# Kernel tuning notes

Hardware: AMD Instinct MI355X
Metric: run time of the kernel (lower is better)

Reference implementation:

```python
import jax, jax.numpy as jnp
import numpy as np

V, D, NH, HD, FF, NL, NLOOPS = 1056, 320, 5, 64, 864, 6, 8
CAP, EPS, THETA = 0.8, 1e-6, 10000.0
B, S = 8, 2048


def rmsnorm(x, w):
    return w * (x * jax.lax.rsqrt(jnp.mean(x * x, axis=-1, keepdims=True) + EPS))


def rotate_half(x):
    x1, x2 = jnp.split(x, 2, axis=-1)
    return jnp.concatenate([-x2, x1], axis=-1)


def rope_tables(seq_len):
    freqs = 1.0 / (THETA ** (jnp.arange(0, HD, 2, dtype=jnp.float32) / HD))  # [HD/2]
    t = jnp.arange(seq_len, dtype=jnp.float32)
    f = jnp.outer(t, freqs)                      # [S, HD/2]
    f = jnp.concatenate([f, f], axis=-1)         # [S, HD]
    return jnp.cos(f), jnp.sin(f)


def setup_inputs() -> dict:
    key = jax.random.key(0)
    ks = jax.random.split(key, 12)
    std = 0.02
    inp = {
        "input_ids": jax.random.randint(ks[0], (B, S), 0, V),
        "iteration": 0,
        "embedding": jax.random.normal(ks[1], (V, D), jnp.float32),
        "iter_emb": jax.random.normal(ks[2], (NLOOPS, D), jnp.float32),
        "attn_norm_w": jnp.ones((NL, D), jnp.float32),
        "Wqkv": jax.random.normal(ks[3], (NL, 3 * D, D), jnp.float32) * std,
        "wo_w": jax.random.normal(ks[4], (NL, D, D), jnp.float32) * std,
        "router_w": jax.random.normal(ks[5], (NL, D), jnp.float32) * std,
        "mlp_norm_w": jnp.ones((NL, D), jnp.float32),
        "gate_w": jax.random.normal(ks[6], (NL, FF, D), jnp.float32) * std,
        "up_w": jax.random.normal(ks[7], (NL, FF, D), jnp.float32) * std,
        "down_w": jax.random.normal(ks[8], (NL, D, FF), jnp.float32) * std,
        "final_norm_w": jnp.ones((D,), jnp.float32),
    }
    return inp


def reference(input_ids, iteration, embedding, iter_emb, attn_norm_w, Wqkv, wo_w,
              router_w, mlp_norm_w, gate_w, up_w, down_w, final_norm_w):
    batch, seq = input_ids.shape
    k = max(1, int(seq * CAP))
    cos, sin = rope_tables(seq)                 # [S, HD]
    cos4 = cos[None, :, None, :]                # [1,S,1,HD]
    sin4 = sin[None, :, None, :]

    x = embedding[input_ids]                    # [B,S,D]
    if iteration < NLOOPS:
        x = x + iter_emb[iteration][None, None, :]

    causal = jnp.tril(jnp.ones((seq, seq), dtype=bool))
    bidx = jnp.arange(batch)[:, None]           # [B,1]

    for l in range(NL):
        # --- attention block ---
        h = rmsnorm(x, attn_norm_w[l])
        qkv = (h @ Wqkv[l].T).reshape(batch, seq, 3, NH, HD)
        q, kk, v = qkv[:, :, 0], qkv[:, :, 1], qkv[:, :, 2]   # [B,S,H,HD]
        q = q * cos4 + rotate_half(q) * sin4
        kk = kk * cos4 + rotate_half(kk) * sin4
        q, kk, v = (t.transpose(0, 2, 1, 3) for t in (q, kk, v))  # [B,H,S,HD]
        scores = jnp.einsum("bhqd,bhkd->bhqk", q, kk) / np.sqrt(HD)
        scores = jnp.where(causal, scores, -jnp.inf)
        attn = jax.nn.softmax(scores, axis=-1)
        out = jnp.einsum("bhqk,bhkd->bhqd", attn, v)
        out = out.transpose(0, 2, 1, 3).reshape(batch, seq, D)
        x = x + out @ wo_w[l].T

        # --- MoD router + SwiGLU MLP on selected tokens ---
        probs = jax.nn.sigmoid(x @ router_w[l])            # [B,S]
        topk_probs, topk_idx = jax.lax.top_k(probs, k)     # [B,K]
        sel = jnp.take_along_axis(x, topk_idx[:, :, None], axis=1)  # [B,K,D]
        hs = rmsnorm(sel, mlp_norm_w[l])
        gate = jax.nn.silu(hs @ gate_w[l].T) * (hs @ up_w[l].T)
        mlp = (gate @ down_w[l].T) * topk_probs[:, :, None]         # [B,K,D]
        x = x.at[bidx, topk_idx].add(mlp)                  # unique idx: add == scatter-set+residual

    return rmsnorm(x, final_norm_w)
```

## Files before the change

kernel.cpp:

```cpp
#include <hip/hip_runtime.h>
#include <hip/hip_bf16.h>
#include <math.h>

#define VSZ 1056
#define DD 320
#define NH 5
#define HD 64
#define FF 864
#define NL 6
#define NLOOPS 8
#define BB 8
#define SL 2048
#define KK 1638
#define EPSF 1e-6f

typedef _Float16 f16x8 __attribute__((ext_vector_type(8)));
typedef _Float16 f16x4 __attribute__((ext_vector_type(4)));
typedef float floatx16 __attribute__((ext_vector_type(16)));

__device__ inline void gll16(const void* g, void* l) {
    __builtin_amdgcn_global_load_lds((const __attribute__((address_space(1))) void*)g,
                                     (__attribute__((address_space(3))) void*)l, 16, 0, 0);
}

__global__ __launch_bounds__(256) void cast4_kernel(const float* __restrict__ s,
        _Float16* __restrict__ d, int n4) {
    int i = blockIdx.x * 256 + threadIdx.x;
    if (i >= n4) return;
    float4 v = ((const float4*)s)[i];
    f16x4 o = { (_Float16)v.x, (_Float16)v.y, (_Float16)v.z, (_Float16)v.w };
    *(f16x4*)(d + (size_t)i * 4) = o;
}

__global__ __launch_bounds__(256) void rope_init_kernel(float2* __restrict__ tab) {
    int i = blockIdx.x * 256 + threadIdx.x;
    int s = i >> 5, j = i & 31;
    float freq = exp2f(-(float)j * 0.4152410118609203f);
    float ang = (float)s * freq;
    tab[i] = make_float2(cosf(ang), sinf(ang));
}

__global__ __launch_bounds__(256) void embed_kernel(const int* __restrict__ ids,
        const int* __restrict__ iter, const float* __restrict__ emb,
        const float* __restrict__ iter_emb, float* __restrict__ x) {
    int i = blockIdx.x * 256 + threadIdx.x;
    int d = i % DD, bs = i / DD;
    float v = emb[(size_t)ids[bs] * DD + d];
    int it = iter[0];
    if (it < NLOOPS) v += iter_emb[it * DD + d];
    x[i] = v;
}

template<typename OT>
__global__ __launch_bounds__(256) void rmsnorm_kernel(const float* __restrict__ x,
        const float* __restrict__ w, OT* __restrict__ out, int nrows) {
    int row = blockIdx.x * 4 + (threadIdx.x >> 6);
    int lane = threadIdx.x & 63;
    if (row >= nrows) return;
    const float* xr = x + (size_t)row * DD;
    float v[5]; float ss = 0.f;
#pragma unroll
    for (int i = 0; i < 5; ++i) { v[i] = xr[lane + i * 64]; ss += v[i] * v[i]; }
#pragma unroll
    for (int o = 32; o > 0; o >>= 1) ss += __shfl_xor(ss, o);
    float r = rsqrtf(ss * (1.f / DD) + EPSF);
    OT* orow = out + (size_t)row * DD;
#pragma unroll
    for (int i = 0; i < 5; ++i) orow[lane + i * 64] = (OT)(w[lane + i * 64] * v[i] * r);
}

__global__ __launch_bounds__(256) void gather_rmsnorm_kernel(const float* __restrict__ x,
        const int* __restrict__ tkidx, const float* __restrict__ w,
        _Float16* __restrict__ out, int nrows) {
    int row = blockIdx.x * 4 + (threadIdx.x >> 6);
    int lane = threadIdx.x & 63;
    if (row >= nrows) return;
    int b = row / KK;
    int t = tkidx[row];
    const float* xr = x + ((size_t)b * SL + t) * DD;
    float v[5]; float ss = 0.f;
#pragma unroll
    for (int i = 0; i < 5; ++i) { v[i] = xr[lane + i * 64]; ss += v[i] * v[i]; }
#pragma unroll
    for (int o = 32; o > 0; o >>= 1) ss += __shfl_xor(ss, o);
    float r = rsqrtf(ss * (1.f / DD) + EPSF);
    _Float16* orow = out + (size_t)row * DD;
#pragma unroll
    for (int i = 0; i < 5; ++i) orow[lane + i * 64] = (_Float16)(w[lane + i * 64] * v[i] * r);
}

__global__ __launch_bounds__(256) void router_kernel(const float* __restrict__ x,
        const float* __restrict__ rw, float* __restrict__ probs, int nrows) {
    int row = blockIdx.x * 4 + (threadIdx.x >> 6);
    int lane = threadIdx.x & 63;
    if (row >= nrows) return;
    const float* xr = x + (size_t)row * DD;
    float ss = 0.f;
#pragma unroll
    for (int i = 0; i < 5; ++i) ss += xr[lane + i * 64] * rw[lane + i * 64];
#pragma unroll
    for (int o = 32; o > 0; o >>= 1) ss += __shfl_xor(ss, o);
    if (lane == 0) probs[row] = 1.f / (1.f + __expf(-ss));
}

__global__ __launch_bounds__(1024) void topk_kernel(const float* __restrict__ probs,
        int* __restrict__ tkidx, float* __restrict__ tkprob) {
    __shared__ int hist[256];
    __shared__ int scn[256];
    __shared__ int outc;
    __shared__ int s_digit, s_rem;
    int b = blockIdx.x, tid = threadIdx.x;
    unsigned long long k0, k1;
    {
        unsigned int f0 = __float_as_uint(probs[b * SL + tid]);
        unsigned int f1 = __float_as_uint(probs[b * SL + tid + 1024]);
        k0 = ((unsigned long long)f0 << 32) | (unsigned int)(2047 - tid);
        k1 = ((unsigned long long)f1 << 32) | (unsigned int)(2047 - (tid + 1024));
    }
    if (tid == 0) outc = 0;
    unsigned long long prefix = 0, pmask = 0;
    int target = KK;
    for (int shift = 56; shift >= 0; shift -= 8) {
        if (tid < 256) hist[tid] = 0;
        __syncthreads();
        bool a0 = (k0 & pmask) == prefix;
        bool a1 = (k1 & pmask) == prefix;
        int d0 = (int)((k0 >> shift) & 255);
        int d1 = (int)((k1 >> shift) & 255);
        if (a0) atomicAdd(&hist[d0], 1);
        if (a1) atomicAdd(&hist[d1], 1);
        __syncthreads();
        if (tid < 64) {
            int h0 = hist[tid * 4], h1 = hist[tid * 4 + 1];
            int h2 = hist[tid * 4 + 2], h3 = hist[tid * 4 + 3];
            int s3 = h3, s2 = h2 + s3, s1 = h1 + s2, s0 = h0 + s1;
            int s = s0;
#pragma unroll
            for (int off = 1; off < 64; off <<= 1) {
                int v = __shfl_down(s, off);
                if (tid + off >= 64) v = 0;
                s += v;
            }
            int A = s - s0;
            scn[tid * 4]     = s0 + A;
            scn[tid * 4 + 1] = s1 + A;
            scn[tid * 4 + 2] = s2 + A;
            scn[tid * 4 + 3] = s3 + A;
        }
        __syncthreads();
        if (tid < 256 && hist[tid] > 0) {
            int S = scn[tid];
            int Sgt = S - hist[tid];
            if (Sgt < target && target <= S) { s_digit = tid; s_rem = target - Sgt; }
        }
        __syncthreads();
        int dsel = s_digit, rem = s_rem;
        bool full = (rem == hist[dsel]);
        if (a0 && (d0 > dsel || (full && d0 == dsel))) {
            int s = atomicAdd(&outc, 1);
            tkidx[b * KK + s] = 2047 - (int)(k0 & 0xffffffffu);
            tkprob[b * KK + s] = __uint_as_float((unsigned int)(k0 >> 32));
        }
        if (a1 && (d1 > dsel || (full && d1 == dsel))) {
            int s = atomicAdd(&outc, 1);
            tkidx[b * KK + s] = 2047 - (int)(k1 & 0xffffffffu);
            tkprob[b * KK + s] = __uint_as_float((unsigned int)(k1 >> 32));
        }
        if (full) break;
        target = rem;
        prefix |= ((unsigned long long)dsel) << shift;
        pmask  |= ((unsigned long long)255) << shift;
        __syncthreads();
    }
}

__global__ __launch_bounds__(256) void prep_kernel(const _Float16* __restrict__ qkv,
        const float2* __restrict__ ropet,
        _Float16* __restrict__ Qh, _Float16* __restrict__ Kt, _Float16* __restrict__ Vt) {
    __shared__ _Float16 vt[64][72];
    int tid = threadIdx.x;
    int t = blockIdx.x, h = blockIdx.y, b = blockIdx.z;
    int bh = b * NH + h;
    int c = tid >> 5;
    int slb = tid & 31;
    const float QS = 0.125f * 1.44269504088896341f;
#pragma unroll
    for (int half = 0; half < 2; ++half) {
        int sl = half * 32 + slb;
        int s = t * 64 + sl;
        size_t rbase = ((size_t)(b * SL + s) * 3) * (NH * 64) + h * 64;
        f16x8 qv = *(const f16x8*)(qkv + rbase + c * 8);
        f16x8 qp = *(const f16x8*)(qkv + rbase + (c ^ 4) * 8);
        f16x8 kv = *(const f16x8*)(qkv + rbase + NH * 64 + c * 8);
        f16x8 kp = *(const f16x8*)(qkv + rbase + NH * 64 + (c ^ 4) * 8);
        f16x8 vv = *(const f16x8*)(qkv + rbase + 2 * NH * 64 + c * 8);
        const float2* rp = ropet + (size_t)s * 32 + (c & 3) * 8;
        f16x8 qo, ko;
#pragma unroll
        for (int j = 0; j < 8; ++j) {
            int d = c * 8 + j;
            float2 cs = rp[j];
            float cc = cs.x, sn = cs.y;
            float a = (float)qv[j], p = (float)qp[j];
            float ka = (float)kv[j], kb2 = (float)kp[j];
            float qr = (d < 32) ? a * cc - p * sn : a * cc + p * sn;
            float kr = (d < 32) ? ka * cc - kb2 * sn : ka * cc + kb2 * sn;
            qo[j] = (_Float16)(qr * QS);
            ko[j] = (_Float16)kr;
        }
        *(f16x8*)(Qh + ((size_t)bh * SL + s) * 64 + c * 8) = qo;
        *(f16x8*)(Kt + (((size_t)bh * 32 + t) * 8 + c) * 512 + sl * 8) = ko;
        *(f16x8*)(&vt[sl][c * 8]) = vv;
    }
    __syncthreads();
#pragma unroll
    for (int gg = 0; gg < 2; ++gg) {
        int oo = tid * 16 + gg * 8;
        int kc = oo >> 9;
        int d = (oo >> 3) & 63;
        f16x8 vo;
#pragma unroll
        for (int j = 0; j < 8; ++j) {
            int key = (kc >> 1) * 16 + (j & 3) + 8 * (j >> 2) + 4 * (kc & 1);
            vo[j] = vt[key][d];
        }
        *(f16x8*)(Vt + (((size_t)bh * 32 + t) * 8 + kc) * 512 + d * 8) = vo;
    }
}

__global__ __launch_bounds__(256, 2) void attn_mfma(const _Float16* __restrict__ Qh,
        const _Float16* __restrict__ Kt, const _Float16* __restrict__ Vt,
        _Float16* __restrict__ attn_out) {
    __shared__ float red[4][32][32];
    __shared__ float msh[4][32];
    __shared__ float lsh[4][32];
    int tid = threadIdx.x;
    int w = tid >> 6;
    int lane = tid & 63;
    int l31 = lane & 31, h5 = lane >> 5;
    int g = blockIdx.x;
    int j = g >> 3;
    int bh = (g & 7) + 8 * (j >> 6);
    int qt = 63 - (j & 63);
    int b = bh / NH, h = bh % NH;
    int nt = (qt >> 1) + 1;
    int qw = qt * 32;
    int myq = qw + l31;

    f16x8 qf[4];
    const _Float16* qrow = Qh + ((size_t)bh * SL + myq) * 64;
#pragma unroll
    for (int kd = 0; kd < 4; ++kd) qf[kd] = *(const f16x8*)(qrow + kd * 16 + h5 * 8);

    const _Float16* Kb = Kt + (size_t)bh * 32 * 4096;
    const _Float16* Vb = Vt + (size_t)bh * 32 * 4096;

    floatx16 O0, O1;
#pragma unroll
    for (int r = 0; r < 16; ++r) { O0[r] = 0.f; O1[r] = 0.f; }
    float m = -INFINITY, l = 0.f;

    for (int t = w; t < nt; t += 4) {
        const _Float16* kb = Kb + (size_t)t * 4096;
        const _Float16* vb = Vb + (size_t)t * 4096;
        f16x8 a0[4], a1[4], v0[4], v1[4];
#pragma unroll
        for (int kd = 0; kd < 4; ++kd) {
            int off = (kd * 2 + h5) * 512 + l31 * 8;
            a0[kd] = *(const f16x8*)(kb + off);
            a1[kd] = *(const f16x8*)(kb + off + 256);
        }
#pragma unroll
        for (int kc = 0; kc < 4; ++kc) {
            int off = (kc * 2 + h5) * 512 + l31 * 8;
            v0[kc] = *(const f16x8*)(vb + off);
            v1[kc] = *(const f16x8*)(vb + off + 256);
        }
        floatx16 S0, S1;
#pragma unroll
        for (int r = 0; r < 16; ++r) { S0[r] = 0.f; S1[r] = 0.f; }
#pragma unroll
        for (int kd = 0; kd < 4; ++kd) {
            S0 = __builtin_amdgcn_mfma_f32_32x32x16_f16(a0[kd], qf[kd], S0, 0, 0, 0);
            S1 = __builtin_amdgcn_mfma_f32_32x32x16_f16(a1[kd], qf[kd], S1, 0, 0, 0);
        }
        int t0 = t * 64;
        if (t0 + 63 > qw) {
#pragma unroll
            for (int r = 0; r < 16; ++r) {
                int key = t0 + (r & 3) + 8 * (r >> 2) + 4 * h5;
                if (key > myq) S0[r] = -INFINITY;
                if (key + 32 > myq) S1[r] = -INFINITY;
            }
        }
        float tmax = S0[0];
#pragma unroll
        for (int r = 1; r < 16; ++r) tmax = fmaxf(tmax, S0[r]);
#pragma unroll
        for (int r = 0; r < 16; ++r) tmax = fmaxf(tmax, S1[r]);
        tmax = fmaxf(tmax, __shfl_xor(tmax, 32));
        if (__any(tmax > m + 8.f)) {
            float mnew = fmaxf(m, tmax);
            float alpha = exp2f(m - mnew);
            l *= alpha; O0 *= alpha; O1 *= alpha; m = mnew;
        }
        float P0[16], P1[16]; float psum = 0.f;
#pragma unroll
        for (int r = 0; r < 16; ++r) { P0[r] = exp2f(S0[r] - m); psum += P0[r]; }
#pragma unroll
        for (int r = 0; r < 16; ++r) { P1[r] = exp2f(S1[r] - m); psum += P1[r]; }
        psum += __shfl_xor(psum, 32);
        l += psum;
#pragma unroll
        for (int sub = 0; sub < 2; ++sub) {
            const float* P = sub ? P1 : P0;
#pragma unroll
            for (int kc = 0; kc < 2; ++kc) {
                auto q01 = __builtin_amdgcn_cvt_pkrtz(P[kc * 8 + 0], P[kc * 8 + 1]);
                auto q23 = __builtin_amdgcn_cvt_pkrtz(P[kc * 8 + 2], P[kc * 8 + 3]);
                auto q45 = __builtin_amdgcn_cvt_pkrtz(P[kc * 8 + 4], P[kc * 8 + 5]);
                auto q67 = __builtin_amdgcn_cvt_pkrtz(P[kc * 8 + 6], P[kc * 8 + 7]);
                f16x8 pf;
                pf[0] = (_Float16)q01[0]; pf[1] = (_Float16)q01[1];
                pf[2] = (_Float16)q23[0]; pf[3] = (_Float16)q23[1];
                pf[4] = (_Float16)q45[0]; pf[5] = (_Float16)q45[1];
                pf[6] = (_Float16)q67[0]; pf[7] = (_Float16)q67[1];
                int ksg = sub * 2 + kc;
                O0 = __builtin_amdgcn_mfma_f32_32x32x16_f16(v0[ksg], pf, O0, 0, 0, 0);
                O1 = __builtin_amdgcn_mfma_f32_32x32x16_f16(v1[ksg], pf, O1, 0, 0, 0);
            }
        }
    }
    if (h5 == 0) msh[w][l31] = m;
    __syncthreads();
    float M = fmaxf(fmaxf(msh[0][l31], msh[1][l31]), fmaxf(msh[2][l31], msh[3][l31]));
    float wgt = exp2f(m - M);
    if (h5 == 0) lsh[w][l31] = l * wgt;
#pragma unroll
    for (int r = 0; r < 16; ++r) {
        int d = (r & 3) + 8 * (r >> 2) + 4 * h5;
        red[w][d][l31] = O0[r] * wgt;
    }
    __syncthreads();
    float lsum = lsh[0][l31] + lsh[1][l31] + lsh[2][l31] + lsh[3][l31];
    float linv = 1.f / lsum;
    if (w < 2) {
        f16x8 ov;
#pragma unroll
        for (int k = 0; k < 8; ++k) {
            int d = w * 16 + h5 * 8 + k;
            ov[k] = (_Float16)((red[0][d][l31] + red[1][d][l31] +
                                red[2][d][l31] + red[3][d][l31]) * linv);
        }
        *(f16x8*)(attn_out + ((size_t)(b * SL + myq)) * DD + h * 64 + w * 16 + h5 * 8) = ov;
    }
    __syncthreads();
#pragma unroll
    for (int r = 0; r < 16; ++r) {
        int d = (r & 3) + 8 * (r >> 2) + 4 * h5;
        red[w][d][l31] = O1[r] * wgt;
    }
    __syncthreads();
    if (w >= 2) {
        f16x8 ov;
#pragma unroll
        for (int k = 0; k < 8; ++k) {
            int d = (w - 2) * 16 + h5 * 8 + k;
            ov[k] = (_Float16)((red[0][d][l31] + red[1][d][l31] +
                                red[2][d][l31] + red[3][d][l31]) * linv);
        }
        *(f16x8*)(attn_out + ((size_t)(b * SL + myq)) * DD + h * 64 + 32 + (w - 2) * 16 + h5 * 8) = ov;
    }
}

template<int MODE>
__global__ __launch_bounds__(256) void gemm_mfma(const _Float16* __restrict__ A,
        const _Float16* __restrict__ W, _Float16* __restrict__ Ch, float* __restrict__ X,
        int M, int N, int K, int nn_tiles, const int* __restrict__ sidx, const float* __restrict__ sprob) {
    __shared__ __attribute__((aligned(16))) _Float16 As[2][2048];
    __shared__ __attribute__((aligned(16))) _Float16 Ws[2][2048];
    int tid = threadIdx.x;
    int lane = tid & 63;
    int wave = tid >> 6;
    int l31 = lane & 31, h5 = lane >> 5;
    int nwg = gridDim.x;
    int q = nwg >> 3, r = nwg & 7;
    int xcd = blockIdx.x & 7, idx = blockIdx.x >> 3;
    int wgid = (xcd < r ? xcd * (q + 1) : r * (q + 1) + (xcd - r) * q) + idx;
    int mt = wgid / nn_tiles;
    int nt = wgid - mt * nn_tiles;
    int m0 = mt * 64, n0 = nt * 64;
    int wm = (wave & 1) * 32, wn = (wave >> 1) * 32;

    int srow = tid & 63;
    int skc = tid >> 6;
    int arow = m0 + srow; if (arow >= M) arow = M - 1;
    int wrow = n0 + srow; if (wrow >= N) wrow = N - 1;
    const _Float16* Ag = A + (size_t)arow * K + skc * 8;
    const _Float16* Wg = W + (size_t)wrow * K + skc * 8;
    _Float16* AsD = As[0] + (size_t)(tid & ~63) * 8;
    _Float16* WsD = Ws[0] + (size_t)(tid & ~63) * 8;

    floatx16 acc;
#pragma unroll
    for (int i = 0; i < 16; ++i) acc[i] = 0.f;

    gll16(Ag, AsD);
    gll16(Wg, WsD);
    __syncthreads();

    int nk = K >> 5;
    for (int t = 0; t < nk; ++t) {
        int buf = t & 1;
        if (t + 1 < nk) {
            int k0 = (t + 1) * 32;
            int bo = (buf ^ 1) * 2048;
            gll16(Ag + k0, AsD + bo);
            gll16(Wg + k0, WsD + bo);
        }
        const _Float16* Asb = As[buf];
        const _Float16* Wsb = Ws[buf];
#pragma unroll
        for (int ks = 0; ks < 2; ++ks) {
            int kc = ks * 2 + h5;
            f16x8 a = *(const f16x8*)(Asb + kc * 512 + (wm + l31) * 8);
            f16x8 b = *(const f16x8*)(Wsb + kc * 512 + (wn + l31) * 8);
            acc = __builtin_amdgcn_mfma_f32_32x32x16_f16(a, b, acc, 0, 0, 0);
        }
        __syncthreads();
    }

    int nn = n0 + wn + l31;
#pragma unroll
    for (int r2 = 0; r2 < 16; ++r2) {
        int mm = m0 + wm + (r2 & 3) + 8 * (r2 >> 2) + 4 * h5;
        if (mm >= M || nn >= N) continue;
        float v = acc[r2];
        if (MODE == 0) {
            Ch[(size_t)mm * N + nn] = (_Float16)v;
        } else if (MODE == 1) {
            X[(size_t)mm * N + nn] += v;
        } else {
            int b = mm / KK;
            X[((size_t)(b * SL + sidx[mm])) * N + nn] += v * sprob[mm];
        }
    }
}

__global__ __launch_bounds__(256) void gemm_gateup(const _Float16* __restrict__ A,
        const _Float16* __restrict__ Wg, const _Float16* __restrict__ Wu,
        _Float16* __restrict__ Ch, int M, int N, int K, int nn_tiles) {
    __shared__ __attribute__((aligned(16))) _Float16 As[2][2048];
    __shared__ __attribute__((aligned(16))) _Float16 Wgs[2][2048];
    __shared__ __attribute__((aligned(16))) _Float16 Wus[2][2048];
    int tid = threadIdx.x;
    int lane = tid & 63;
    int wave = tid >> 6;
    int l31 = lane & 31, h5 = lane >> 5;
    int nwg = gridDim.x;
    int q = nwg >> 3, r = nwg & 7;
    int xcd = blockIdx.x & 7, idx = blockIdx.x >> 3;
    int wgid = (xcd < r ? xcd * (q + 1) : r * (q + 1) + (xcd - r) * q) + idx;
    int mt = wgid / nn_tiles;
    int nt = wgid - mt * nn_tiles;
    int m0 = mt * 64, n0 = nt * 64;
    int wm = (wave & 1) * 32, wn = (wave >> 1) * 32;

    int srow = tid & 63;
    int skc = tid >> 6;
    int arow = m0 + srow; if (arow >= M) arow = M - 1;
    int wrow = n0 + srow; if (wrow >= N) wrow = N - 1;
    const _Float16* Ag  = A  + (size_t)arow * K + skc * 8;
    const _Float16* Wgg = Wg + (size_t)wrow * K + skc * 8;
    const _Float16* Wug = Wu + (size_t)wrow * K + skc * 8;
    _Float16* AsD  = As[0]  + (size_t)(tid & ~63) * 8;
    _Float16* WgsD = Wgs[0] + (size_t)(tid & ~63) * 8;
    _Float16* WusD = Wus[0] + (size_t)(tid & ~63) * 8;

    floatx16 ag, au;
#pragma unroll
    for (int i = 0; i < 16; ++i) { ag[i] = 0.f; au[i] = 0.f; }

    gll16(Ag, AsD);
    gll16(Wgg, WgsD);
    gll16(Wug, WusD);
    __syncthreads();

    int nk = K >> 5;
    for (int t = 0; t < nk; ++t) {
        int buf = t & 1;
        if (t + 1 < nk) {
            int k0 = (t + 1) * 32;
            int bo = (buf ^ 1) * 2048;
            gll16(Ag + k0, AsD + bo);
            gll16(Wgg + k0, WgsD + bo);
            gll16(Wug + k0, WusD + bo);
        }
        const _Float16* Asb = As[buf];
        const _Float16* Wgb = Wgs[buf];
        const _Float16* Wub = Wus[buf];
#pragma unroll
        for (int ks = 0; ks < 2; ++ks) {
            int kc = ks * 2 + h5;
            f16x8 a  = *(const f16x8*)(Asb + kc * 512 + (wm + l31) * 8);
            f16x8 g0 = *(const f16x8*)(Wgb + kc * 512 + (wn + l31) * 8);
            f16x8 u0 = *(const f16x8*)(Wub + kc * 512 + (wn + l31) * 8);
            ag = __builtin_amdgcn_mfma_f32_32x32x16_f16(a, g0, ag, 0, 0, 0);
            au = __builtin_amdgcn_mfma_f32_32x32x16_f16(a, u0, au, 0, 0, 0);
        }
        __syncthreads();
    }

    int nn = n0 + wn + l31;
#pragma unroll
    for (int r2 = 0; r2 < 16; ++r2) {
        int mm = m0 + wm + (r2 & 3) + 8 * (r2 >> 2) + 4 * h5;
        if (mm >= M || nn >= N) continue;
        float gv = ag[r2], uv = au[r2];
        Ch[(size_t)mm * N + nn] = (_Float16)((gv / (1.f + __expf(-gv))) * uv);
    }
}

extern "C" void kernel_launch(void* const* d_in, const int* in_sizes, int n_in,
                              void* d_out, int out_size, void* d_ws, size_t ws_size,
                              hipStream_t stream) {
    const int*   ids          = (const int*)d_in[0];
    const int*   iter         = (const int*)d_in[1];
    const float* emb          = (const float*)d_in[2];
    const float* iter_emb     = (const float*)d_in[3];
    const float* attn_norm_w  = (const float*)d_in[4];
    const float* Wqkv         = (const float*)d_in[5];
    const float* wo_w         = (const float*)d_in[6];
    const float* router_w     = (const float*)d_in[7];
    const float* mlp_norm_w   = (const float*)d_in[8];
    const float* gate_w       = (const float*)d_in[9];
    const float* up_w         = (const float*)d_in[10];
    const float* down_w       = (const float*)d_in[11];
    const float* final_norm_w = (const float*)d_in[12];
    float* out = (float*)d_out;

    const size_t XN   = (size_t)BB * SL * DD;
    const size_t QKVN = (size_t)BB * SL * 3 * DD;
    const size_t HN   = (size_t)BB * NH * SL * 64;
    char* ws = (char*)d_ws;
    size_t off = 0;
    float*    x        = (float*)(ws + off);    off += XN * 4;
    _Float16* h        = (_Float16*)(ws + off); off += XN * 2;
    _Float16* attn_out = (_Float16*)(ws + off); off += XN * 2;
    float*    probs    = (float*)(ws + off);    off += (size_t)BB * SL * 4;
    int*      tkidx    = (int*)(ws + off);      off += (size_t)BB * KK * 4;
    float*    tkprob   = (float*)(ws + off);    off += (size_t)BB * KK * 4;
    off = (off + 255) & ~(size_t)255;
    _Float16* qkvh     = (_Float16*)(ws + off); off += QKVN * 2;
    _Float16* Qh       = (_Float16*)(ws + off); off += HN * 2;
    _Float16* Kh       = (_Float16*)(ws + off); off += HN * 2;
    _Float16* Vh       = (_Float16*)(ws + off); off += HN * 2;
    float2*   ropet    = (float2*)(ws + off);   off += (size_t)SL * 32 * 8;
    _Float16* WqkvH    = (_Float16*)(ws + off);
    _Float16* woH   = WqkvH + (size_t)NL * 3 * DD * DD;
    _Float16* gateH = woH   + (size_t)NL * DD * DD;
    _Float16* upH   = gateH + (size_t)NL * FF * DD;
    _Float16* downH = upH   + (size_t)NL * FF * DD;
    _Float16* g1 = qkvh;

    rope_init_kernel<<<SL * 32 / 256, 256, 0, stream>>>(ropet);
    cast4_kernel<<<(NL * 3 * DD * DD / 4 + 255) / 256, 256, 0, stream>>>(Wqkv, WqkvH, NL * 3 * DD * DD / 4);
    cast4_kernel<<<(NL * DD * DD / 4 + 255) / 256, 256, 0, stream>>>(wo_w, woH, NL * DD * DD / 4);
    cast4_kernel<<<(NL * FF * DD / 4 + 255) / 256, 256, 0, stream>>>(gate_w, gateH, NL * FF * DD / 4);
    cast4_kernel<<<(NL * FF * DD / 4 + 255) / 256, 256, 0, stream>>>(up_w, upH, NL * FF * DD / 4);
    cast4_kernel<<<(NL * DD * FF / 4 + 255) / 256, 256, 0, stream>>>(down_w, downH, NL * DD * FF / 4);

    embed_kernel<<<20480, 256, 0, stream>>>(ids, iter, emb, iter_emb, x);

    const int M1 = BB * SL;
    const int M2 = BB * KK;
    const int MT1 = (M1 + 63) / 64;
    const int MT2 = (M2 + 63) / 64;
    for (int l = 0; l < NL; ++l) {
        rmsnorm_kernel<_Float16><<<4096, 256, 0, stream>>>(x, attn_norm_w + l * DD, h, M1);
        gemm_mfma<0><<<MT1 * 15, 256, 0, stream>>>(h, WqkvH + (size_t)l * 3 * DD * DD,
                                                   qkvh, nullptr, M1, 3 * DD, DD, 15, nullptr, nullptr);
        prep_kernel<<<dim3(SL / 64, NH, BB), 256, 0, stream>>>(qkvh, ropet, Qh, Kh, Vh);
        attn_mfma<<<BB * NH * (SL / 32), 256, 0, stream>>>(Qh, Kh, Vh, attn_out);
        gemm_mfma<1><<<MT1 * 5, 256, 0, stream>>>(attn_out, woH + (size_t)l * DD * DD,
                                                  nullptr, x, M1, DD, DD, 5, nullptr, nullptr);
        router_kernel<<<4096, 256, 0, stream>>>(x, router_w + l * DD, probs, M1);
        topk_kernel<<<BB, 1024, 0, stream>>>(probs, tkidx, tkprob);
        gather_rmsnorm_kernel<<<3276, 256, 0, stream>>>(x, tkidx, mlp_norm_w + l * DD, h, M2);
        gemm_gateup<<<MT2 * 14, 256, 0, stream>>>(h, gateH + (size_t)l * FF * DD,
                                                  upH + (size_t)l * FF * DD, g1, M2, FF, DD, 14);
        gemm_mfma<2><<<MT2 * 5, 256, 0, stream>>>(g1, downH + (size_t)l * DD * FF,
                                                  nullptr, x, M2, DD, FF, 5, tkidx, tkprob);
    }
    rmsnorm_kernel<float><<<4096, 256, 0, stream>>>(x, final_norm_w, out, M1);
}
```

Baseline: 1.547 ms.

## Widen GEMM N-tiles to 128 for QKV and gate/up, deepen K-step to 64

Adds a dedicated QKV GEMM and changes the gate/up GEMM so each block computes a 64x128 output tile with two accumulators per wave. This reuses each loaded A tile across twice as many output columns and halves the number of workgroups. The generic gemm_mfma now stages 64 K-elements per barrier, with a tail path for odd K/32. The cost is more LDS and registers per block and fewer blocks per launch, which may reduce occupancy.

```diff
diff --git a/kernel.cpp b/kernel.cpp
--- a/kernel.cpp
+++ b/kernel.cpp
@@ -373,12 +373,86 @@
     }
 }
 
+__global__ __launch_bounds__(256) void gemm_qkv(const _Float16* __restrict__ A,
+        const _Float16* __restrict__ W, _Float16* __restrict__ Ch,
+        int M, int N, int K, int nn_tiles) {
+    __shared__ __attribute__((aligned(16))) _Float16 As[2][2048];
+    __shared__ __attribute__((aligned(16))) _Float16 Ws[2][4096];
+    int tid = threadIdx.x;
+    int lane = tid & 63;
+    int wave = tid >> 6;
+    int l31 = lane & 31, h5 = lane >> 5;
+    int nwg = gridDim.x;
+    int q = nwg >> 3, r = nwg & 7;
+    int xcd = blockIdx.x & 7, idx = blockIdx.x >> 3;
+    int wgid = (xcd < r ? xcd * (q + 1) : r * (q + 1) + (xcd - r) * q) + idx;
+    int mt = wgid / nn_tiles;
+    int nt = wgid - mt * nn_tiles;
+    int m0 = mt * 64, n0 = nt * 128;
+    int wm = (wave & 1) * 32, wn2 = (wave >> 1) * 64;
+
+    int srA = tid & 63, skA = tid >> 6;
+    int srW = tid & 127, skW = tid >> 7;
+    int arow = m0 + srA; if (arow >= M) arow = M - 1;
+    int wrow = n0 + srW; if (wrow >= N) wrow = N - 1;
+    const _Float16* Ag = A + (size_t)arow * K + skA * 8;
+    const _Float16* Wg = W + (size_t)wrow * K + skW * 8;
+    _Float16* AsD = As[0] + (size_t)(tid & ~63) * 8;
+    _Float16* WsD = Ws[0] + (size_t)(tid & ~63) * 8;
+
+    floatx16 acc0, acc1;
+#pragma unroll
+    for (int i = 0; i < 16; ++i) { acc0[i] = 0.f; acc1[i] = 0.f; }
+
+    gll16(Ag, AsD);
+    gll16(Wg, WsD);
+    gll16(Wg + 16, WsD + 2048);
+    __syncthreads();
+
+    int nk = K >> 5;
+    for (int t = 0; t < nk; ++t) {
+        int buf = t & 1;
+        if (t + 1 < nk) {
+            int k0 = (t + 1) * 32;
+            int bo = buf ^ 1;
+            gll16(Ag + k0, AsD + bo * 2048);
+            gll16(Wg + k0, WsD + bo * 4096);
+            gll16(Wg + k0 + 16, WsD + bo * 4096 + 2048);
+        }
+        const _Float16* Asb = As[buf];
+        const _Float16* Wsb = Ws[buf];
+#pragma unroll
+        for (int ks = 0; ks < 2; ++ks) {
+            int kc = ks * 2 + h5;
+            f16x8 a  = *(const f16x8*)(Asb + kc * 512 + (wm + l31) * 8);
+            f16x8 b0 = *(const f16x8*)(Wsb + kc * 1024 + (wn2 + l31) * 8);
+            f16x8 b1 = *(const f16x8*)(Wsb + kc * 1024 + (wn2 + 32 + l31) * 8);
+            acc0 = __builtin_amdgcn_mfma_f32_32x32x16_f16(a, b0, acc0, 0, 0, 0);
+            acc1 = __builtin_amdgcn_mfma_f32_32x32x16_f16(a, b1, acc1, 0, 0, 0);
+        }
+        __syncthreads();
+    }
+
+#pragma unroll
+    for (int nj = 0; nj < 2; ++nj) {
+        int nn = n0 + wn2 + nj * 32 + l31;
+        if (nn >= N) continue;
+        const floatx16& ac = nj ? acc1 : acc0;
+#pragma unroll
+        for (int r2 = 0; r2 < 16; ++r2) {
+            int mm = m0 + wm + (r2 & 3) + 8 * (r2 >> 2) + 4 * h5;
+            if (mm >= M) continue;
+            Ch[(size_t)mm * N + nn] = (_Float16)ac[r2];
+        }
+    }
+}
+
 template<int MODE>
 __global__ __launch_bounds__(256) void gemm_mfma(const _Float16* __restrict__ A,
         const _Float16* __restrict__ W, _Float16* __restrict__ Ch, float* __restrict__ X,
         int M, int N, int K, int nn_tiles, const int* __restrict__ sidx, const float* __restrict__ sprob) {
-    __shared__ __attribute__((aligned(16))) _Float16 As[2][2048];
-    __shared__ __attribute__((aligned(16))) _Float16 Ws[2][2048];
+    __shared__ __attribute__((aligned(16))) _Float16 As[2][4096];
+    __shared__ __attribute__((aligned(16))) _Float16 Ws[2][4096];
     int tid = threadIdx.x;
     int lane = tid & 63;
     int wave = tid >> 6;
@@ -405,19 +479,43 @@
 #pragma unroll
     for (int i = 0; i < 16; ++i) acc[i] = 0.f;
 
+    int nk32 = K >> 5;
+    int nfull = nk32 >> 1;
+    int tail = nk32 & 1;
+
     gll16(Ag, AsD);
     gll16(Wg, WsD);
+    gll16(Ag + 32, AsD + 2048);
+    gll16(Wg + 32, WsD + 2048);
     __syncthreads();
 
-    int nk = K >> 5;
-    for (int t = 0; t < nk; ++t) {
+    for (int t = 0; t < nfull; ++t) {
         int buf = t & 1;
-        if (t + 1 < nk) {
-            int k0 = (t + 1) * 32;
-            int bo = (buf ^ 1) * 2048;
+        int bo = (buf ^ 1) * 4096;
+        if (t + 1 < nfull) {
+            int k0 = (t + 1) * 64;
             gll16(Ag + k0, AsD + bo);
             gll16(Wg + k0, WsD + bo);
-        }
+            gll16(Ag + k0 + 32, AsD + bo + 2048);
+            gll16(Wg + k0 + 32, WsD + bo + 2048);
+        } else if (tail) {
+            int k0 = nfull * 64;
+            gll16(Ag + k0, AsD + bo);
+            gll16(Wg + k0, WsD + bo);
+        }
+        const _Float16* Asb = As[buf];
+        const _Float16* Wsb = Ws[buf];
+#pragma unroll
+        for (int ks = 0; ks < 4; ++ks) {
+            int kc = ks * 2 + h5;
+            f16x8 a = *(const f16x8*)(Asb + kc * 512 + (wm + l31) * 8);
+            f16x8 b = *(const f16x8*)(Wsb + kc * 512 + (wn + l31) * 8);
+            acc = __builtin_amdgcn_mfma_f32_32x32x16_f16(a, b, acc, 0, 0, 0);
+        }
+        __syncthreads();
+    }
+    if (tail) {
+        int buf = nfull & 1;
         const _Float16* Asb = As[buf];
         const _Float16* Wsb = Ws[buf];
 #pragma unroll
@@ -427,7 +525,6 @@
             f16x8 b = *(const f16x8*)(Wsb + kc * 512 + (wn + l31) * 8);
             acc = __builtin_amdgcn_mfma_f32_32x32x16_f16(a, b, acc, 0, 0, 0);
         }
-        __syncthreads();
     }
 
     int nn = n0 + wn + l31;
@@ -436,9 +533,7 @@
         int mm = m0 + wm + (r2 & 3) + 8 * (r2 >> 2) + 4 * h5;
         if (mm >= M || nn >= N) continue;
         float v = acc[r2];
-        if (MODE == 0) {
-            Ch[(size_t)mm * N + nn] = (_Float16)v;
-        } else if (MODE == 1) {
+        if (MODE == 1) {
             X[(size_t)mm * N + nn] += v;
         } else {
             int b = mm / KK;
@@ -451,8 +546,8 @@
         const _Float16* __restrict__ Wg, const _Float16* __restrict__ Wu,
         _Float16* __restrict__ Ch, int M, int N, int K, int nn_tiles) {
     __shared__ __attribute__((aligned(16))) _Float16 As[2][2048];
-    __shared__ __attribute__((aligned(16))) _Float16 Wgs[2][2048];
-    __shared__ __attribute__((aligned(16))) _Float16 Wus[2][2048];
+    __shared__ __attribute__((aligned(16))) _Float16 Wgs[2][4096];
+    __shared__ __attribute__((aligned(16))) _Float16 Wus[2][4096];
     int tid = threadIdx.x;
     int lane = tid & 63;
     int wave = tid >> 6;
@@ -463,27 +558,29 @@
     int wgid = (xcd < r ? xcd * (q + 1) : r * (q + 1) + (xcd - r) * q) + idx;
     int mt = wgid / nn_tiles;
     int nt = wgid - mt * nn_tiles;
-    int m0 = mt * 64, n0 = nt * 64;
-    int wm = (wave & 1) * 32, wn = (wave >> 1) * 32;
-
-    int srow = tid & 63;
-    int skc = tid >> 6;
-    int arow = m0 + srow; if (arow >= M) arow = M - 1;
-    int wrow = n0 + srow; if (wrow >= N) wrow = N - 1;
-    const _Float16* Ag  = A  + (size_t)arow * K + skc * 8;
-    const _Float16* Wgg = Wg + (size_t)wrow * K + skc * 8;
-    const _Float16* Wug = Wu + (size_t)wrow * K + skc * 8;
+    int m0 = mt * 64, n0 = nt * 128;
+    int wm = (wave & 1) * 32, wn2 = (wave >> 1) * 64;
+
+    int srA = tid & 63, skA = tid >> 6;
+    int srW = tid & 127, skW = tid >> 7;
+    int arow = m0 + srA; if (arow >= M) arow = M - 1;
+    int wrow = n0 + srW; if (wrow >= N) wrow = N - 1;
+    const _Float16* Ag  = A  + (size_t)arow * K + skA * 8;
+    const _Float16* Wgg = Wg + (size_t)wrow * K + skW * 8;
+    const _Float16* Wug = Wu + (size_t)wrow * K + skW * 8;
     _Float16* AsD  = As[0]  + (size_t)(tid & ~63) * 8;
     _Float16* WgsD = Wgs[0] + (size_t)(tid & ~63) * 8;
     _Float16* WusD = Wus[0] + (size_t)(tid & ~63) * 8;
 
-    floatx16 ag, au;
-#pragma unroll
-    for (int i = 0; i < 16; ++i) { ag[i] = 0.f; au[i] = 0.f; }
+    floatx16 ag0, ag1, au0, au1;
+#pragma unroll
+    for (int i = 0; i < 16; ++i) { ag0[i] = 0.f; ag1[i] = 0.f; au0[i] = 0.f; au1[i] = 0.f; }
 
     gll16(Ag, AsD);
     gll16(Wgg, WgsD);
+    gll16(Wgg + 16, WgsD + 2048);
     gll16(Wug, WusD);
+    gll16(Wug + 16, WusD + 2048);
     __syncthreads();
 
     int nk = K >> 5;
@@ -491,10 +588,12 @@
         int buf = t & 1;
         if (t + 1 < nk) {
             int k0 = (t + 1) * 32;
-            int bo = (buf ^ 1) * 2048;
-            gll16(Ag + k0, AsD + bo);
-            gll16(Wgg + k0, WgsD + bo);
-            gll16(Wug + k0, WusD + bo);
+            int bo = buf ^ 1;
+            gll16(Ag + k0, AsD + bo * 2048);
+            gll16(Wgg + k0, WgsD + bo * 4096);
+            gll16(Wgg + k0 + 16, WgsD + bo * 4096 + 2048);
+            gll16(Wug + k0, WusD + bo * 4096);
+            gll16(Wug + k0 + 16, WusD + bo * 4096 + 2048);
         }
         const _Float16* Asb = As[buf];
         const _Float16* Wgb = Wgs[buf];
@@ -503,21 +602,31 @@
         for (int ks = 0; ks < 2; ++ks) {
             int kc = ks * 2 + h5;
             f16x8 a  = *(const f16x8*)(Asb + kc * 512 + (wm + l31) * 8);
-            f16x8 g0 = *(const f16x8*)(Wgb + kc * 512 + (wn + l31) * 8);
-            f16x8 u0 = *(const f16x8*)(Wub + kc * 512 + (wn + l31) * 8);
-            ag = __builtin_amdgcn_mfma_f32_32x32x16_f16(a, g0, ag, 0, 0, 0);
-            au = __builtin_amdgcn_mfma_f32_32x32x16_f16(a, u0, au, 0, 0, 0);
+            f16x8 g0 = *(const f16x8*)(Wgb + kc * 1024 + (wn2 + l31) * 8);
+            f16x8 g1 = *(const f16x8*)(Wgb + kc * 1024 + (wn2 + 32 + l31) * 8);
+            f16x8 u0 = *(const f16x8*)(Wub + kc * 1024 + (wn2 + l31) * 8);
+            f16x8 u1 = *(const f16x8*)(Wub + kc * 1024 + (wn2 + 32 + l31) * 8);
+            ag0 = __builtin_amdgcn_mfma_f32_32x32x16_f16(a, g0, ag0, 0, 0, 0);
+            au0 = __builtin_amdgcn_mfma_f32_32x32x16_f16(a, u0, au0, 0, 0, 0);
+            ag1 = __builtin_amdgcn_mfma_f32_32x32x16_f16(a, g1, ag1, 0, 0, 0);
+            au1 = __builtin_amdgcn_mfma_f32_32x32x16_f16(a, u1, au1, 0, 0, 0);
         }
         __syncthreads();
     }
 
-    int nn = n0 + wn + l31;
-#pragma unroll
-    for (int r2 = 0; r2 < 16; ++r2) {
-        int mm = m0 + wm + (r2 & 3) + 8 * (r2 >> 2) + 4 * h5;
-        if (mm >= M || nn >= N) continue;
-        float gv = ag[r2], uv = au[r2];
-        Ch[(size_t)mm * N + nn] = (_Float16)((gv / (1.f + __expf(-gv))) * uv);
+#pragma unroll
+    for (int nj = 0; nj < 2; ++nj) {
+        int nn = n0 + wn2 + nj * 32 + l31;
+        if (nn >= N) continue;
+        const floatx16& gA = nj ? ag1 : ag0;
+        const floatx16& uA = nj ? au1 : au0;
+#pragma unroll
+        for (int r2 = 0; r2 < 16; ++r2) {
+            int mm = m0 + wm + (r2 & 3) + 8 * (r2 >> 2) + 4 * h5;
+            if (mm >= M) continue;
+            float gv = gA[r2], uv = uA[r2];
+            Ch[(size_t)mm * N + nn] = (_Float16)((gv / (1.f + __expf(-gv))) * uv);
+        }
     }
 }
 
@@ -578,8 +687,8 @@
     const int MT2 = (M2 + 63) / 64;
     for (int l = 0; l < NL; ++l) {
         rmsnorm_kernel<_Float16><<<4096, 256, 0, stream>>>(x, attn_norm_w + l * DD, h, M1);
-        gemm_mfma<0><<<MT1 * 15, 256, 0, stream>>>(h, WqkvH + (size_t)l * 3 * DD * DD,
-                                                   qkvh, nullptr, M1, 3 * DD, DD, 15, nullptr, nullptr);
+        gemm_qkv<<<MT1 * 8, 256, 0, stream>>>(h, WqkvH + (size_t)l * 3 * DD * DD,
+                                              qkvh, M1, 3 * DD, DD, 8);
         prep_kernel<<<dim3(SL / 64, NH, BB), 256, 0, stream>>>(qkvh, ropet, Qh, Kh, Vh);
         attn_mfma<<<BB * NH * (SL / 32), 256, 0, stream>>>(Qh, Kh, Vh, attn_out);
         gemm_mfma<1><<<MT1 * 5, 256, 0, stream>>>(attn_out, woH + (size_t)l * DD * DD,
@@ -587,8 +696,8 @@
         router_kernel<<<4096, 256, 0, stream>>>(x, router_w + l * DD, probs, M1);
         topk_kernel<<<BB, 1024, 0, stream>>>(probs, tkidx, tkprob);
         gather_rmsnorm_kernel<<<3276, 256, 0, stream>>>(x, tkidx, mlp_norm_w + l * DD, h, M2);
-        gemm_gateup<<<MT2 * 14, 256, 0, stream>>>(h, gateH + (size_t)l * FF * DD,
-                                                  upH + (size_t)l * FF * DD, g1, M2, FF, DD, 14);
+        gemm_gateup<<<MT2 * 7, 256, 0, stream>>>(h, gateH + (size_t)l * FF * DD,
+                                                 upH + (size_t)l * FF * DD, g1, M2, FF, DD, 7);
         gemm_mfma<2><<<MT2 * 5, 256, 0, stream>>>(g1, downH + (size_t)l * DD * FF,
                                                   nullptr, x, M2, DD, FF, 5, tkidx, tkprob);
     }
```

After: 1.538 ms (median of 2 runs). Within noise of the previous version (-0.6%).
